# Optimization experiments

Hardware: AMD Instinct MI355X
Metric: run time of the kernel (lower is better)

Reference implementation:

```python
import jax, jax.numpy as jnp
import numpy as np

TILE = 16


def _quat_to_rotmat(q):
    # q: [N,4] (r,x,y,z), normalized first (torch.nn.functional.normalize semantics)
    q = q / jnp.linalg.norm(q, axis=-1, keepdims=True)
    r, x, y, z = q[:, 0], q[:, 1], q[:, 2], q[:, 3]
    R = jnp.stack([
        1 - 2 * (y * y + z * z), 2 * (x * y - r * z), 2 * (x * z + r * y),
        2 * (x * y + r * z), 1 - 2 * (x * x + z * z), 2 * (y * z - r * x),
        2 * (x * z - r * y), 2 * (y * z + r * x), 1 - 2 * (x * x + y * y),
    ], axis=-1).reshape(-1, 3, 3)
    return R


def _forward(xyz, scaling, rotation, opacity, rot, res):
    N = xyz.shape[0]
    xy_mean = xyz[:, :2] * (res / 2.0)                      # [N,2]

    # cov2d: L = R @ diag(raw scaling); cov3d = L L^T; S = diag(W,H,0)
    R = _quat_to_rotmat(rotation)                            # [N,3,3]
    L = R * scaling[:, None, :]                              # [N,3,3]
    cov3d = L @ jnp.swapaxes(L, 1, 2)                        # [N,3,3]
    S = jnp.diag(jnp.array([res, res, 0.0], dtype=xyz.dtype))
    A = S @ rot                                              # [3,3]
    cov2d = jnp.einsum('ij,njk,lk->nil', A, cov3d, A)[:, :2, :2]  # [N,2,2]
    c00, c01 = cov2d[:, 0, 0], cov2d[:, 0, 1]
    c10, c11 = cov2d[:, 1, 0], cov2d[:, 1, 1]

    # radius = ceil(3 * sqrt(max eigenvalue)) with standard 3DGS clamp
    det = c00 * c11 - c01 * c10
    mid = 0.5 * (c00 + c11)
    sq = jnp.sqrt(jnp.maximum(mid * mid - det, 0.1))
    radii = jnp.ceil(3.0 * jnp.sqrt(jnp.maximum(mid + sq, mid - sq)))  # [N]

    # rect (torch-splatting get_rect): clip corners to [0, res-1]
    rmin = jnp.clip(xy_mean - radii[:, None], 0.0, res - 1.0)          # [N,2]
    rmax = jnp.clip(xy_mean + radii[:, None], 0.0, res - 1.0)

    # tile/gaussian overlap mask (replicates the python double loop's in_mask)
    nt = res // TILE
    tstart = (jnp.arange(nt) * TILE).astype(xyz.dtype)                 # [nt]
    mask_x = jnp.minimum(rmax[None, :, 0], tstart[:, None] + TILE - 1) > \
             jnp.maximum(rmin[None, :, 0], tstart[:, None])            # [nt,N]
    mask_y = jnp.minimum(rmax[None, :, 1], tstart[:, None] + TILE - 1) > \
             jnp.maximum(rmin[None, :, 1], tstart[:, None])            # [nt,N]
    mask = mask_y[:, None, :] & mask_x[None, :, :]                     # [nt_h,nt_w,N]
    maskpix = jnp.repeat(jnp.repeat(mask, TILE, axis=0), TILE, axis=1)
    maskpix = maskpix.reshape(res * res, N).astype(xyz.dtype)          # [P,N]

    # pixel grid, meshgrid(x, y, indexing='xy'): pixel (i,j) -> (x[j], y[i])
    coords = jnp.linspace(-res / 2.0, res / 2.0 - 1.0, res, dtype=xyz.dtype) + 0.5
    px = jnp.tile(coords, res)      # [P] x varies fastest
    py = jnp.repeat(coords, res)    # [P]

    # conic = cov2d^{-1} (analytic 2x2 inverse)
    idet = 1.0 / det
    i00, i11 = c11 * idet, c00 * idet
    i01, i10 = -c01 * idet, -c10 * idet

    dx0 = px[:, None] - xy_mean[None, :, 0]                            # [P,N]
    dx1 = py[:, None] - xy_mean[None, :, 1]                            # [P,N]
    power = -0.5 * (dx0 * dx0 * i00 + dx1 * dx1 * i11 + dx0 * dx1 * (i01 + i10))
    w = jnp.exp(power)                                                 # [P,N]

    # alpha = sum_n w * raw_opacity, masked by tile overlap
    acc = jnp.einsum('pn,pn,n->p', w, maskpix, opacity[:, 0])
    return acc.reshape(res, res, 1)


def setup_inputs() -> dict:
    key = jax.random.key(0)
    k1, k2, k3, k4, k5 = jax.random.split(key, 5)
    N, res = 1024, 256
    return {
        'xyz': jax.random.uniform(k1, (N, 3), dtype=jnp.float32),
        'scaling': jax.random.uniform(k2, (N, 3), dtype=jnp.float32),
        'rotation': jax.random.normal(k3, (N, 4), dtype=jnp.float32),
        'opacity': jax.random.uniform(k4, (N, 1), dtype=jnp.float32),
        'rot': jax.random.normal(k5, (3, 3), dtype=jnp.float32),
        'res': res,
    }


def reference(xyz, scaling, rotation, opacity, rot, res):
    return _forward(xyz, scaling, rotation, opacity, rot, res)
```

## Files before the change

### kernel.cpp

```cpp
#include <hip/hip_runtime.h>
#include <math.h>


#define TILE 16
#define MAXG 1024
#define NW   16
#define GPW  (MAXG / NW)

__global__ __launch_bounds__(1024, 1) void gs_fused(
    const float* __restrict__ xyz, const float* __restrict__ scaling,
    const float* __restrict__ rotation, const float* __restrict__ opacity,
    const float* __restrict__ rot, float* __restrict__ out,
    int N, int res, int nt)
{
    __shared__ float4 sP[MAXG];
    __shared__ float2 sQ[MAXG];
    __shared__ float4 sR[NW][64];

    const int tid = threadIdx.x;
    const int w = tid >> 6, l = tid & 63;
    const int tX = blockIdx.x % nt, tY = blockIdx.x / nt;
    const float resf = (float)res;

    const int px0 = tX * TILE + (l & 7) * 2;
    const int py0 = tY * TILE + (l >> 3) * 2;
    const float ctr = resf * 0.5f - 0.5f;
    const float Xa = (float)px0 - ctr, Xb = Xa + 1.f;
    const float Ya = (float)py0 - ctr, Yb = Ya + 1.f;
    const float XaYa = Xa * Ya;
    const float sXab = Xa + Xb;
    const float sYab = Ya + Yb;

    const float tx0 = (float)(tX * TILE), tx1 = tx0 + (float)(TILE - 1);
    const float ty0 = (float)(tY * TILE), ty1 = ty0 + (float)(TILE - 1);

    float acc00 = 0.f, acc10 = 0.f, acc01 = 0.f, acc11 = 0.f;

    for (int base = 0; base < N; base += MAXG) {
        const int C = min(MAXG, N - base);

        for (int slot = tid; slot < MAXG; slot += 1024) {
            float4 P = make_float4(0.f, 0.f, 0.f, 0.f);
            float2 Q = make_float2(0.f, -INFINITY);
            if (slot < C) {
                int n = base + slot;
                float qr = rotation[4*n+0], qx = rotation[4*n+1];
                float qy = rotation[4*n+2], qz = rotation[4*n+3];
                float inv = 1.0f / sqrtf(qr*qr + qx*qx + qy*qy + qz*qz);
                float r = qr*inv, x = qx*inv, y = qy*inv, z = qz*inv;

                float R00 = 1.f - 2.f*(y*y + z*z), R01 = 2.f*(x*y - r*z), R02 = 2.f*(x*z + r*y);
                float R10 = 2.f*(x*y + r*z), R11 = 1.f - 2.f*(x*x + z*z), R12 = 2.f*(y*z - r*x);
                float R20 = 2.f*(x*z - r*y), R21 = 2.f*(y*z + r*x), R22 = 1.f - 2.f*(x*x + y*y);

                float s0 = scaling[3*n+0], s1 = scaling[3*n+1], s2 = scaling[3*n+2];
                float L00 = R00*s0, L01 = R01*s1, L02 = R02*s2;
                float L10 = R10*s0, L11 = R11*s1, L12 = R12*s2;
                float L20 = R20*s0, L21 = R21*s1, L22 = R22*s2;

                float a00 = resf*rot[0], a01 = resf*rot[1], a02 = resf*rot[2];
                float a10 = resf*rot[3], a11 = resf*rot[4], a12 = resf*rot[5];
                float b00 = a00*L00 + a01*L10 + a02*L20;
                float b01 = a00*L01 + a01*L11 + a02*L21;
                float b02 = a00*L02 + a01*L12 + a02*L22;
                float b10 = a10*L00 + a11*L10 + a12*L20;
                float b11 = a10*L01 + a11*L11 + a12*L21;
                float b12 = a10*L02 + a11*L12 + a12*L22;
                float c00 = b00*b00 + b01*b01 + b02*b02;
                float c01 = b00*b10 + b01*b11 + b02*b12;
                float c11 = b10*b10 + b11*b11 + b12*b12;

                float det = c00*c11 - c01*c01;
                float mid = 0.5f*(c00 + c11);
                float sq  = sqrtf(fmaxf(mid*mid - det, 0.1f));
                float lam = fmaxf(mid + sq, mid - sq);
                float radii = ceilf(3.0f * sqrtf(lam));

                float mx = xyz[3*n+0] * (resf*0.5f);
                float my = xyz[3*n+1] * (resf*0.5f);
                float rminx = fminf(fmaxf(mx - radii, 0.f), resf - 1.f);
                float rmaxx = fminf(fmaxf(mx + radii, 0.f), resf - 1.f);
                float rminy = fminf(fmaxf(my - radii, 0.f), resf - 1.f);
                float rmaxy = fminf(fmaxf(my + radii, 0.f), resf - 1.f);

                bool pass = (fminf(rmaxx, tx1) > fmaxf(rminx, tx0)) &&
                            (fminf(rmaxy, ty1) > fmaxf(rminy, ty0));

                float idet = 1.0f / det;
                const float L2E = 1.44269504088896340736f;
                float A  = -0.5f * L2E * c11 * idet;
                float B  = -0.5f * L2E * c00 * idet;
                float Cc =         L2E * c01 * idet;

                float c3 = -2.f*A*mx - Cc*my;
                float c4 = -2.f*B*my - Cc*mx;
                float c5 = A*mx*mx + B*my*my + Cc*mx*my + log2f(opacity[n]);

                P = make_float4(A, B, Cc, c3);
                Q = make_float2(c4, pass ? c5 : -INFINITY);
            }
            sP[slot] = P;
            sQ[slot] = Q;
        }
        __syncthreads();

        const int g0 = w * GPW;
        #pragma unroll 4
        for (int i = g0; i < g0 + GPW; ++i) {
            float4 p  = sP[i];
            float2 qv = sQ[i];
            float t1  = fmaf(p.x, Xa, p.w);
            float t3  = fmaf(p.y, Ya, qv.x);
            float t2  = fmaf(t1, Xa, qv.y);
            float t4  = fmaf(t3, Ya, t2);
            float qaa = fmaf(p.z, XaYa, t4);
            float dx0 = fmaf(p.x, sXab, p.w);
            float dy0 = fmaf(p.y, sYab, qv.x);
            float dX  = fmaf(p.z, Ya, dx0);
            float dY  = fmaf(p.z, Xa, dy0);
            float qba = qaa + dX;
            float qab = qaa + dY;
            float qbb = qab + (dX + p.z);
            acc00 += __builtin_amdgcn_exp2f(qaa);
            acc10 += __builtin_amdgcn_exp2f(qba);
            acc01 += __builtin_amdgcn_exp2f(qab);
            acc11 += __builtin_amdgcn_exp2f(qbb);
        }
        __syncthreads();
    }

    sR[w][l] = make_float4(acc00, acc10, acc01, acc11);
    __syncthreads();
    if (w == 0) {
        float4 s = sR[0][l];
        #pragma unroll
        for (int k = 1; k < NW; ++k) {
            float4 t = sR[k][l];
            s.x += t.x; s.y += t.y; s.z += t.z; s.w += t.w;
        }
        float* o = out + py0 * res + px0;
        *(float2*)(o)       = make_float2(s.x, s.y);
        *(float2*)(o + res) = make_float2(s.z, s.w);
    }
}

extern "C" void kernel_launch(void* const* d_in, const int* in_sizes, int n_in,
                              void* d_out, int out_size, void* d_ws, size_t ws_size,
                              hipStream_t stream) {
    const float* xyz      = (const float*)d_in[0];
    const float* scaling  = (const float*)d_in[1];
    const float* rotation = (const float*)d_in[2];
    const float* opacity  = (const float*)d_in[3];
    const float* rot      = (const float*)d_in[4];
    int N   = in_sizes[0] / 3;
    int res = (int)(sqrt((double)out_size) + 0.5);
    int nt  = res / TILE;

    float* out = (float*)d_out;

    gs_fused<<<dim3(nt * nt), 1024, 0, stream>>>(
        xyz, scaling, rotation, opacity, rot, out, N, res, nt);
}
```

Before: 19.60 us.

## Broadcast per-Gaussian params via readlane instead of shared memory

```diff
diff --git a/kernel.cpp b/kernel.cpp
--- a/kernel.cpp
+++ b/kernel.cpp
@@ -3,9 +3,13 @@
 
 
 #define TILE 16
-#define MAXG 1024
-#define NW   16
-#define GPW  (MAXG / NW)
+#define NW    16
+#define CHUNK 1024
+
+__device__ __forceinline__ float rlane(float v, int lane) {
+    return __uint_as_float(
+        (unsigned)__builtin_amdgcn_readlane((int)__float_as_uint(v), lane));
+}
 
 __global__ __launch_bounds__(1024, 1) void gs_fused(
     const float* __restrict__ xyz, const float* __restrict__ scaling,
@@ -13,8 +17,6 @@
     const float* __restrict__ rot, float* __restrict__ out,
     int N, int res, int nt)
 {
-    __shared__ float4 sP[MAXG];
-    __shared__ float2 sQ[MAXG];
     __shared__ float4 sR[NW][64];
 
     const int tid = threadIdx.x;
@@ -25,108 +27,104 @@
     const int px0 = tX * TILE + (l & 7) * 2;
     const int py0 = tY * TILE + (l >> 3) * 2;
     const float ctr = resf * 0.5f - 0.5f;
-    const float Xa = (float)px0 - ctr, Xb = Xa + 1.f;
-    const float Ya = (float)py0 - ctr, Yb = Ya + 1.f;
-    const float XaYa = Xa * Ya;
-    const float sXab = Xa + Xb;
-    const float sYab = Ya + Yb;
+    const float Xa = (float)px0 - ctr;
+    const float Ya = (float)py0 - ctr;
+    const float Xa2 = Xa * Xa, Ya2 = Ya * Ya, XaYa = Xa * Ya;
+    const float sXab = 2.f * Xa + 1.f;
+    const float sYab = 2.f * Ya + 1.f;
 
     const float tx0 = (float)(tX * TILE), tx1 = tx0 + (float)(TILE - 1);
     const float ty0 = (float)(tY * TILE), ty1 = ty0 + (float)(TILE - 1);
 
     float acc00 = 0.f, acc10 = 0.f, acc01 = 0.f, acc11 = 0.f;
 
-    for (int base = 0; base < N; base += MAXG) {
-        const int C = min(MAXG, N - base);
+    for (int base = 0; base < N; base += CHUNK) {
+        float cA = 0.f, cB = 0.f, cC = 0.f, cc3 = 0.f, cc4 = 0.f, cc5 = -INFINITY;
+        int n = base + tid;
+        if (n < N) {
+            float qr = rotation[4*n+0], qx = rotation[4*n+1];
+            float qy = rotation[4*n+2], qz = rotation[4*n+3];
+            float inv = 1.0f / sqrtf(qr*qr + qx*qx + qy*qy + qz*qz);
+            float r = qr*inv, x = qx*inv, y = qy*inv, z = qz*inv;
 
-        for (int slot = tid; slot < MAXG; slot += 1024) {
-            float4 P = make_float4(0.f, 0.f, 0.f, 0.f);
-            float2 Q = make_float2(0.f, -INFINITY);
-            if (slot < C) {
-                int n = base + slot;
-                float qr = rotation[4*n+0], qx = rotation[4*n+1];
-                float qy = rotation[4*n+2], qz = rotation[4*n+3];
-                float inv = 1.0f / sqrtf(qr*qr + qx*qx + qy*qy + qz*qz);
-                float r = qr*inv, x = qx*inv, y = qy*inv, z = qz*inv;
+            float R00 = 1.f - 2.f*(y*y + z*z), R01 = 2.f*(x*y - r*z), R02 = 2.f*(x*z + r*y);
+            float R10 = 2.f*(x*y + r*z), R11 = 1.f - 2.f*(x*x + z*z), R12 = 2.f*(y*z - r*x);
+            float R20 = 2.f*(x*z - r*y), R21 = 2.f*(y*z + r*x), R22 = 1.f - 2.f*(x*x + y*y);
 
-                float R00 = 1.f - 2.f*(y*y + z*z), R01 = 2.f*(x*y - r*z), R02 = 2.f*(x*z + r*y);
-                float R10 = 2.f*(x*y + r*z), R11 = 1.f - 2.f*(x*x + z*z), R12 = 2.f*(y*z - r*x);
-                float R20 = 2.f*(x*z - r*y), R21 = 2.f*(y*z + r*x), R22 = 1.f - 2.f*(x*x + y*y);
+            float s0 = scaling[3*n+0], s1 = scaling[3*n+1], s2 = scaling[3*n+2];
+            float L00 = R00*s0, L01 = R01*s1, L02 = R02*s2;
+            float L10 = R10*s0, L11 = R11*s1, L12 = R12*s2;
+            float L20 = R20*s0, L21 = R21*s1, L22 = R22*s2;
 
-                float s0 = scaling[3*n+0], s1 = scaling[3*n+1], s2 = scaling[3*n+2];
-                float L00 = R00*s0, L01 = R01*s1, L02 = R02*s2;
-                float L10 = R10*s0, L11 = R11*s1, L12 = R12*s2;
-                float L20 = R20*s0, L21 = R21*s1, L22 = R22*s2;
+            float a00 = resf*rot[0], a01 = resf*rot[1], a02 = resf*rot[2];
+            float a10 = resf*rot[3], a11 = resf*rot[4], a12 = resf*rot[5];
+            float b00 = a00*L00 + a01*L10 + a02*L20;
+            float b01 = a00*L01 + a01*L11 + a02*L21;
+            float b02 = a00*L02 + a01*L12 + a02*L22;
+            float b10 = a10*L00 + a11*L10 + a12*L20;
+            float b11 = a10*L01 + a11*L11 + a12*L21;
+            float b12 = a10*L02 + a11*L12 + a12*L22;
+            float c00 = b00*b00 + b01*b01 + b02*b02;
+            float c01 = b00*b10 + b01*b11 + b02*b12;
+            float c11 = b10*b10 + b11*b11 + b12*b12;
 
-                float a00 = resf*rot[0], a01 = resf*rot[1], a02 = resf*rot[2];
-                float a10 = resf*rot[3], a11 = resf*rot[4], a12 = resf*rot[5];
-                float b00 = a00*L00 + a01*L10 + a02*L20;
-                float b01 = a00*L01 + a01*L11 + a02*L21;
-                float b02 = a00*L02 + a01*L12 + a02*L22;
-                float b10 = a10*L00 + a11*L10 + a12*L20;
-                float b11 = a10*L01 + a11*L11 + a12*L21;
-                float b12 = a10*L02 + a11*L12 + a12*L22;
-                float c00 = b00*b00 + b01*b01 + b02*b02;
-                float c01 = b00*b10 + b01*b11 + b02*b12;
-                float c11 = b10*b10 + b11*b11 + b12*b12;
+            float det = c00*c11 - c01*c01;
+            float mid = 0.5f*(c00 + c11);
+            float sq  = sqrtf(fmaxf(mid*mid - det, 0.1f));
+            float lam = fmaxf(mid + sq, mid - sq);
+            float radii = ceilf(3.0f * sqrtf(lam));
 
-                float det = c00*c11 - c01*c01;
-                float mid = 0.5f*(c00 + c11);
-                float sq  = sqrtf(fmaxf(mid*mid - det, 0.1f));
-                float lam = fmaxf(mid + sq, mid - sq);
-                float radii = ceilf(3.0f * sqrtf(lam));
+            float mx = xyz[3*n+0] * (resf*0.5f);
+            float my = xyz[3*n+1] * (resf*0.5f);
+            float rminx = fminf(fmaxf(mx - radii, 0.f), resf - 1.f);
+            float rmaxx = fminf(fmaxf(mx + radii, 0.f), resf - 1.f);
+            float rminy = fminf(fmaxf(my - radii, 0.f), resf - 1.f);
+            float rmaxy = fminf(fmaxf(my + radii, 0.f), resf - 1.f);
 
-                float mx = xyz[3*n+0] * (resf*0.5f);
-                float my = xyz[3*n+1] * (resf*0.5f);
-                float rminx = fminf(fmaxf(mx - radii, 0.f), resf - 1.f);
-                float rmaxx = fminf(fmaxf(mx + radii, 0.f), resf - 1.f);
-                float rminy = fminf(fmaxf(my - radii, 0.f), resf - 1.f);
-                float rmaxy = fminf(fmaxf(my + radii, 0.f), resf - 1.f);
+            bool pass = (fminf(rmaxx, tx1) > fmaxf(rminx, tx0)) &&
+                        (fminf(rmaxy, ty1) > fmaxf(rminy, ty0));
 
-                bool pass = (fminf(rmaxx, tx1) > fmaxf(rminx, tx0)) &&
-                            (fminf(rmaxy, ty1) > fmaxf(rminy, ty0));
+            float idet = 1.0f / det;
+            const float L2E = 1.44269504088896340736f;
+            cA = -0.5f * L2E * c11 * idet;
+            cB = -0.5f * L2E * c00 * idet;
+            cC =         L2E * c01 * idet;
 
-                float idet = 1.0f / det;
-                const float L2E = 1.44269504088896340736f;
-                float A  = -0.5f * L2E * c11 * idet;
-                float B  = -0.5f * L2E * c00 * idet;
-                float Cc =         L2E * c01 * idet;
+            cc3 = -2.f*cA*mx - cC*my;
+            cc4 = -2.f*cB*my - cC*mx;
+            float c5 = cA*mx*mx + cB*my*my + cC*mx*my + log2f(opacity[n]);
+            cc5 = pass ? c5 : -INFINITY;
+        }
 
-                float c3 = -2.f*A*mx - Cc*my;
-                float c4 = -2.f*B*my - Cc*mx;
-                float c5 = A*mx*mx + B*my*my + Cc*mx*my + log2f(opacity[n]);
-
-                P = make_float4(A, B, Cc, c3);
-                Q = make_float2(c4, pass ? c5 : -INFINITY);
-            }
-            sP[slot] = P;
-            sQ[slot] = Q;
-        }
-        __syncthreads();
-
-        const int g0 = w * GPW;
-        #pragma unroll 4
-        for (int i = g0; i < g0 + GPW; ++i) {
-            float4 p  = sP[i];
-            float2 qv = sQ[i];
-            float t1  = fmaf(p.x, Xa, p.w);
-            float t3  = fmaf(p.y, Ya, qv.x);
-            float t2  = fmaf(t1, Xa, qv.y);
-            float t4  = fmaf(t3, Ya, t2);
-            float qaa = fmaf(p.z, XaYa, t4);
-            float dx0 = fmaf(p.x, sXab, p.w);
-            float dy0 = fmaf(p.y, sYab, qv.x);
-            float dX  = fmaf(p.z, Ya, dx0);
-            float dY  = fmaf(p.z, Xa, dy0);
+        #pragma unroll
+        for (int i = 0; i < 64; ++i) {
+            float A  = rlane(cA,  i);
+            float B  = rlane(cB,  i);
+            float C  = rlane(cC,  i);
+            float s3 = rlane(cc3, i);
+            float s4 = rlane(cc4, i);
+            float s5 = rlane(cc5, i);
+            float t0  = A * Xa2;
+            float t1  = fmaf(B, Ya2, t0);
+            float t2  = fmaf(C, XaYa, t1);
+            float t3  = fmaf(s3, Xa, t2);
+            float t4  = fmaf(s4, Ya, t3);
+            float qaa = t4 + s5;
+            float d0  = A * sXab;
+            float d1  = fmaf(C, Ya, d0);
+            float dX  = d1 + s3;
+            float e0  = B * sYab;
+            float e1  = fmaf(C, Xa, e0);
+            float dY  = e1 + s4;
             float qba = qaa + dX;
             float qab = qaa + dY;
-            float qbb = qab + (dX + p.z);
+            float dX2 = dX + C;
+            float qbb = qab + dX2;
             acc00 += __builtin_amdgcn_exp2f(qaa);
             acc10 += __builtin_amdgcn_exp2f(qba);
             acc01 += __builtin_amdgcn_exp2f(qab);
             acc11 += __builtin_amdgcn_exp2f(qbb);
         }
-        __syncthreads();
     }
 
     sR[w][l] = make_float4(acc00, acc10, acc01, acc11);
```

Result: slower. 21.01 us (+7.2%).
